# Performance work log

Hardware: AMD Instinct MI355X
Metric: run time of the kernel (lower is better)

## Reference

```python
import jax, jax.numpy as jnp
import numpy as np

EMB = 384
GROUPS = 4
B, T = 32, 1024
MAX_DUR = 8
SILENCE_VAL = -11.5129251


def setup_inputs() -> dict:
    key = jax.random.key(0)
    k1, k2, k3, k4, k5 = jax.random.split(key, 5)
    phoneme = jax.random.normal(k1, (B, T, EMB), dtype=jnp.float32)
    durations = jax.random.randint(k2, (B, T + 1), 0, MAX_DUR, dtype=jnp.int32)
    t_out = int(np.asarray(jnp.sum(durations, axis=-1)).max())
    silence_token = jnp.full((EMB,), SILENCE_VAL, dtype=jnp.float32)
    # DurationPredictor params (grouped conv -> ReLU -> 1x1 conv to scalar)
    conv1_w = jax.random.normal(k3, (EMB, EMB // GROUPS, 3), dtype=jnp.float32) * 0.05
    conv1_b = jnp.zeros((EMB,), dtype=jnp.float32)
    conv2_w = jax.random.normal(k4, (1, EMB, 1), dtype=jnp.float32) * 0.05
    conv2_b = jnp.zeros((1,), dtype=jnp.float32)
    return {
        "phoneme": phoneme,
        "silence_token": silence_token,
        "conv1_w": conv1_w,
        "conv1_b": conv1_b,
        "conv2_w": conv2_w,
        "conv2_b": conv2_b,
        "durations": durations,
        "t_out": t_out,
    }


def _duration_predictor(x, conv1_w, conv1_b, conv2_w, conv2_b):
    # x: [B, Tp, E] -> durations_pred [B, Tp]
    xc = jnp.transpose(x, (0, 2, 1))  # [B, E, Tp]
    h = jax.lax.conv_general_dilated(
        xc, conv1_w, window_strides=(1,), padding=((1, 1),),
        dimension_numbers=("NCH", "OIH", "NCH"), feature_group_count=GROUPS)
    h = jax.nn.relu(h + conv1_b[None, :, None])
    d = jax.lax.conv_general_dilated(
        h, conv2_w, window_strides=(1,), padding=((0, 0),),
        dimension_numbers=("NCH", "OIH", "NCH"))
    return d[:, 0, :] + conv2_b[0]  # [B, Tp]


def _regulate(phoneme, durations, t_out):
    # Equivalent to the one-hot mask matmul: frame t gets token j where
    # cumsum[j-1] <= t < cumsum[j]; frames past total length are zero.
    cum = jnp.cumsum(durations, axis=-1)  # [B, Tp]
    pos = jnp.arange(t_out, dtype=cum.dtype)  # [t_out]
    idx = jax.vmap(lambda c: jnp.searchsorted(c, pos, side="right"))(cum)  # [B, t_out]
    valid = pos[None, :] < cum[:, -1:]
    idx = jnp.clip(idx, 0, phoneme.shape[1] - 1)
    gathered = jnp.take_along_axis(phoneme, idx[..., None], axis=1)  # [B, t_out, E]
    return jnp.where(valid[..., None], gathered, jnp.zeros((), phoneme.dtype))


def reference(phoneme, silence_token, conv1_w, conv1_b, conv2_w, conv2_b, durations, t_out):
    Bn = phoneme.shape[0]
    silence = jnp.broadcast_to(silence_token[None, None, :], (Bn, 1, phoneme.shape[2]))
    ph = jnp.concatenate((phoneme, silence), axis=1)  # [B, T+1, E]
    durations_pred = _duration_predictor(ph, conv1_w, conv1_b, conv2_w, conv2_b)
    expanded = _regulate(ph, durations, t_out)  # [B, t_out, E]
    return expanded, durations_pred
```

## Files before the change

### kernel.cpp

```cpp
#include <hip/hip_runtime.h>

#define BATCH 32
#define T_IN 1024
#define TP 1025
#define EMB 384
#define GROUPS 4
#define GC 96
#define KDIM 288

typedef __attribute__((ext_vector_type(8))) short short8;
typedef __attribute__((ext_vector_type(4))) float f32x4;

#define N_WPACK (GROUPS * 9 * 6 * 64 * 8)

__device__ __forceinline__ unsigned short f2bf(float f) {
    union { float f; unsigned u; } v; v.f = f;
    unsigned u = v.u + 0x7fffu + ((v.u >> 16) & 1u);
    return (unsigned short)(u >> 16);
}

__global__ __launch_bounds__(256) void prep_kernel(const float* __restrict__ w1,
                                                   const float* __restrict__ b2,
                                                   unsigned short* __restrict__ wpack,
                                                   float* __restrict__ pred) {
    int i = blockIdx.x * 256 + threadIdx.x;
    if (i < N_WPACK) {
        int j = i & 7;
        int lane = (i >> 3) & 63;
        int rest = i >> 9;
        int nt = rest % 6; rest /= 6;
        int ks = rest % 9;
        int g = rest / 9;
        int oc = nt * 16 + (lane & 15);
        int kk = ks * 32 + (lane >> 4) * 8 + j;
        int k = kk / 96, ic = kk % 96;
        float v = w1[((size_t)(g * GC + oc) * GC + ic) * 3 + k];
        wpack[i] = f2bf(v);
    }
    if (i < BATCH * TP) pred[i] = b2[0];
}

__global__ __launch_bounds__(64) void scan_kernel(const int* __restrict__ dur,
                                                  int* __restrict__ cum) {
    const int b = blockIdx.x;
    const int l = threadIdx.x;
    const int* d = dur + b * TP;
    int* c = cum + b * TP;
    int offset = 0;
    for (int r = 0; r < 17; ++r) {
        int idx = r * 64 + l;
        int v = (idx < TP) ? d[idx] : 0;
        int s = v;
#pragma unroll
        for (int off = 1; off < 64; off <<= 1) {
            int n = __shfl_up(s, off, 64);
            if (l >= off) s += n;
        }
        if (idx < TP) c[idx] = s + offset;
        offset += __shfl(s, 63, 64);
    }
}

__global__ __launch_bounds__(256) void conv_mfma_kernel(const float* __restrict__ phoneme,
                                                        const float* __restrict__ silence,
                                                        const float* __restrict__ b1,
                                                        const float* __restrict__ w2,
                                                        const unsigned short* __restrict__ wpack,
                                                        float* __restrict__ pred) {
    const int tile = blockIdx.x;
    const int g = blockIdx.y;
    const int b = blockIdx.z;
    const int t0 = tile * 64;

    __shared__ __align__(16) unsigned short xs[66][104];
    __shared__ float red[4][16][17];

    const int tid = threadIdx.x;

    for (int e = tid; e < 66 * 24; e += 256) {
        int row = e / 24;
        int v = e - row * 24;
        int r = t0 - 1 + row;
        float4 val;
        if (r < 0 || r > T_IN) {
            val = make_float4(0.f, 0.f, 0.f, 0.f);
        } else if (r == T_IN) {
            val = *(const float4*)(silence + g * GC + v * 4);
        } else {
            val = *(const float4*)(phoneme + ((size_t)(b * T_IN + r)) * EMB + g * GC + v * 4);
        }
        ushort4 pk;
        pk.x = f2bf(val.x); pk.y = f2bf(val.y); pk.z = f2bf(val.z); pk.w = f2bf(val.w);
        *(ushort4*)&xs[row][v * 4] = pk;
    }
    __syncthreads();

    const int w = tid >> 6;
    const int lane = tid & 63;
    const int quad = lane >> 4;
    const int lr = lane & 15;

    f32x4 acc[6];
#pragma unroll
    for (int nt = 0; nt < 6; ++nt) acc[nt] = (f32x4){0.f, 0.f, 0.f, 0.f};

    const unsigned short* wg = wpack + (size_t)g * 9 * 6 * 512;

#pragma unroll
    for (int ks = 0; ks < 9; ++ks) {
        const int k = ks / 3;
        const int icoff = 32 * (ks % 3) + quad * 8;
        const int lrow = w * 16 + lr + k;
        short8 a = *(const short8*)&xs[lrow][icoff];
#pragma unroll
        for (int nt = 0; nt < 6; ++nt) {
            short8 bf = *(const short8*)(wg + ((size_t)(ks * 6 + nt) * 64 + lane) * 8);
            acc[nt] = __builtin_amdgcn_mfma_f32_16x16x32_bf16(a, bf, acc[nt], 0, 0, 0);
        }
    }

    float s[4] = {0.f, 0.f, 0.f, 0.f};
#pragma unroll
    for (int nt = 0; nt < 6; ++nt) {
        int oc = g * GC + nt * 16 + lr;
        float bias = b1[oc];
        float wc = w2[oc];
#pragma unroll
        for (int reg = 0; reg < 4; ++reg) {
            float h = acc[nt][reg] + bias;
            h = h > 0.f ? h : 0.f;
            s[reg] += wc * h;
        }
    }
#pragma unroll
    for (int reg = 0; reg < 4; ++reg) red[w][quad * 4 + reg][lr] = s[reg];
    __syncthreads();

    if (tid < 64) {
        int wv = tid >> 4, m = tid & 15;
        float sum = 0.f;
#pragma unroll
        for (int c2 = 0; c2 < 16; ++c2) sum += red[wv][m][c2];
        int t = t0 + wv * 16 + m;
        if (t < TP) atomicAdd(pred + b * TP + t, sum);
    }
}

__global__ __launch_bounds__(256) void gather_kernel(const float* __restrict__ phoneme,
                                                     const float* __restrict__ silence,
                                                     const int* __restrict__ cum,
                                                     float* __restrict__ out,
                                                     int t_out) {
    const int b = blockIdx.y;
    const int f0 = blockIdx.x * 64;
    const int tid = threadIdx.x;

    __shared__ int sidx[64];
    __shared__ int stotal;

    if (tid == 0) stotal = cum[b * TP + T_IN];
    if (tid < 64) {
        int t = f0 + tid;
        int id = 0;
        if (t < t_out) {
            const int* c = cum + b * TP;
            int lo = 0, hi = TP;
            while (lo < hi) {
                int mid = (lo + hi) >> 1;
                if (c[mid] <= t) lo = mid + 1; else hi = mid;
            }
            id = lo > T_IN ? T_IN : lo;
        }
        sidx[tid] = id;
    }
    __syncthreads();

    const int total = stotal;
    const float4* ph4 = (const float4*)phoneme;
    const float4* s4 = (const float4*)silence;
    float4* out4 = (float4*)out;

    for (int e = tid; e < 64 * 96; e += 256) {
        int fl = e / 96;
        int v = e - fl * 96;
        int t = f0 + fl;
        if (t >= t_out) continue;
        float4 val;
        if (t >= total) {
            val = make_float4(0.f, 0.f, 0.f, 0.f);
        } else {
            int id = sidx[fl];
            val = (id == T_IN) ? s4[v] : ph4[((size_t)(b * T_IN) + id) * 96 + v];
        }
        out4[((size_t)b * t_out + t) * 96 + v] = val;
    }
}

extern "C" void kernel_launch(void* const* d_in, const int* in_sizes, int n_in,
                              void* d_out, int out_size, void* d_ws, size_t ws_size,
                              hipStream_t stream) {
    const float* phoneme = (const float*)d_in[0];
    const float* silence = (const float*)d_in[1];
    const float* conv1_w = (const float*)d_in[2];
    const float* conv1_b = (const float*)d_in[3];
    const float* conv2_w = (const float*)d_in[4];
    const float* conv2_b = (const float*)d_in[5];
    const int* durations = (const int*)d_in[6];
    const int t_out = (out_size - BATCH * TP) / (BATCH * EMB);

    float* out_expanded = (float*)d_out;
    float* out_pred = (float*)d_out + (size_t)BATCH * t_out * EMB;

    int* cum = (int*)d_ws;
    unsigned short* wpack = (unsigned short*)((char*)d_ws + 131200);

    prep_kernel<<<(N_WPACK + 255) / 256, 256, 0, stream>>>(conv1_w, conv2_b, wpack, out_pred);
    scan_kernel<<<BATCH, 64, 0, stream>>>(durations, cum);
    conv_mfma_kernel<<<dim3(17, GROUPS, BATCH), 256, 0, stream>>>(
        phoneme, silence, conv1_b, conv2_w, wpack, out_pred);
    gather_kernel<<<dim3((t_out + 63) / 64, BATCH), 256, 0, stream>>>(
        phoneme, silence, cum, out_expanded, t_out);
}
```

Before: 263.3 us.

## Merge launches into setup and interleaved conv/gather kernel with nontemporal stores

Combines the weight-pack and scan kernels into one setup launch, and merges the conv and gather kernels into one launch whose blocks alternate between conv and gather work. This removes two kernel launches and lets compute-bound conv blocks overlap with bandwidth-bound gather blocks. The scan now preloads all of its duration values into registers before running, and the gather output uses nontemporal stores to avoid polluting the cache. The merged kernel reserves shared memory for both roles, which may lower occupancy.

```diff
diff --git a/kernel.cpp b/kernel.cpp
--- a/kernel.cpp
+++ b/kernel.cpp
@@ -12,6 +12,8 @@
 typedef __attribute__((ext_vector_type(4))) float f32x4;
 
 #define N_WPACK (GROUPS * 9 * 6 * 64 * 8)
+#define PREP_BLOCKS ((N_WPACK + 255) / 256)
+#define CONV_BLOCKS (17 * GROUPS * BATCH)
 
 __device__ __forceinline__ unsigned short f2bf(float f) {
     union { float f; unsigned u; } v; v.f = f;
@@ -19,180 +21,200 @@
     return (unsigned short)(u >> 16);
 }
 
-__global__ __launch_bounds__(256) void prep_kernel(const float* __restrict__ w1,
-                                                   const float* __restrict__ b2,
-                                                   unsigned short* __restrict__ wpack,
-                                                   float* __restrict__ pred) {
-    int i = blockIdx.x * 256 + threadIdx.x;
-    if (i < N_WPACK) {
-        int j = i & 7;
-        int lane = (i >> 3) & 63;
-        int rest = i >> 9;
-        int nt = rest % 6; rest /= 6;
-        int ks = rest % 9;
-        int g = rest / 9;
-        int oc = nt * 16 + (lane & 15);
-        int kk = ks * 32 + (lane >> 4) * 8 + j;
-        int k = kk / 96, ic = kk % 96;
-        float v = w1[((size_t)(g * GC + oc) * GC + ic) * 3 + k];
-        wpack[i] = f2bf(v);
+__global__ __launch_bounds__(256) void setup_kernel(const float* __restrict__ w1,
+                                                    const float* __restrict__ b2,
+                                                    const int* __restrict__ dur,
+                                                    unsigned short* __restrict__ wpack,
+                                                    float* __restrict__ pred,
+                                                    int* __restrict__ cum) {
+    const int bid = blockIdx.x;
+    if (bid < PREP_BLOCKS) {
+        int i = bid * 256 + threadIdx.x;
+        if (i < N_WPACK) {
+            int j = i & 7;
+            int lane = (i >> 3) & 63;
+            int rest = i >> 9;
+            int nt = rest % 6; rest /= 6;
+            int ks = rest % 9;
+            int g = rest / 9;
+            int oc = nt * 16 + (lane & 15);
+            int kk = ks * 32 + (lane >> 4) * 8 + j;
+            int k = kk / 96, ic = kk % 96;
+            float v = w1[((size_t)(g * GC + oc) * GC + ic) * 3 + k];
+            wpack[i] = f2bf(v);
+        }
+        if (i < BATCH * TP) pred[i] = b2[0];
+    } else {
+        const int b = bid - PREP_BLOCKS;
+        const int l = threadIdx.x;
+        if (l >= 64) return;
+        const int* d = dur + b * TP;
+        int* c = cum + b * TP;
+        int v[17];
+#pragma unroll
+        for (int r = 0; r < 17; ++r) {
+            int idx = r * 64 + l;
+            v[r] = (idx < TP) ? d[idx] : 0;
+        }
+        int offset = 0;
+#pragma unroll
+        for (int r = 0; r < 17; ++r) {
+            int s = v[r];
+#pragma unroll
+            for (int off = 1; off < 64; off <<= 1) {
+                int n = __shfl_up(s, off, 64);
+                if (l >= off) s += n;
+            }
+            int idx = r * 64 + l;
+            if (idx < TP) c[idx] = s + offset;
+            offset += __shfl(s, 63, 64);
+        }
     }
-    if (i < BATCH * TP) pred[i] = b2[0];
-}
-
-__global__ __launch_bounds__(64) void scan_kernel(const int* __restrict__ dur,
-                                                  int* __restrict__ cum) {
-    const int b = blockIdx.x;
-    const int l = threadIdx.x;
-    const int* d = dur + b * TP;
-    int* c = cum + b * TP;
-    int offset = 0;
-    for (int r = 0; r < 17; ++r) {
-        int idx = r * 64 + l;
-        int v = (idx < TP) ? d[idx] : 0;
-        int s = v;
-#pragma unroll
-        for (int off = 1; off < 64; off <<= 1) {
-            int n = __shfl_up(s, off, 64);
-            if (l >= off) s += n;
-        }
-        if (idx < TP) c[idx] = s + offset;
-        offset += __shfl(s, 63, 64);
-    }
-}
-
-__global__ __launch_bounds__(256) void conv_mfma_kernel(const float* __restrict__ phoneme,
-                                                        const float* __restrict__ silence,
-                                                        const float* __restrict__ b1,
-                                                        const float* __restrict__ w2,
-                                                        const unsigned short* __restrict__ wpack,
-                                                        float* __restrict__ pred) {
-    const int tile = blockIdx.x;
-    const int g = blockIdx.y;
-    const int b = blockIdx.z;
-    const int t0 = tile * 64;
-
+}
+
+__global__ __launch_bounds__(256) void main_kernel(const float* __restrict__ phoneme,
+                                                   const float* __restrict__ silence,
+                                                   const float* __restrict__ b1,
+                                                   const float* __restrict__ w2,
+                                                   const unsigned short* __restrict__ wpack,
+                                                   const int* __restrict__ cum,
+                                                   float* __restrict__ pred,
+                                                   float* __restrict__ out,
+                                                   int t_out, int nfb, int n_gather) {
     __shared__ __align__(16) unsigned short xs[66][104];
     __shared__ float red[4][16][17];
-
-    const int tid = threadIdx.x;
-
-    for (int e = tid; e < 66 * 24; e += 256) {
-        int row = e / 24;
-        int v = e - row * 24;
-        int r = t0 - 1 + row;
-        float4 val;
-        if (r < 0 || r > T_IN) {
-            val = make_float4(0.f, 0.f, 0.f, 0.f);
-        } else if (r == T_IN) {
-            val = *(const float4*)(silence + g * GC + v * 4);
-        } else {
-            val = *(const float4*)(phoneme + ((size_t)(b * T_IN + r)) * EMB + g * GC + v * 4);
-        }
-        ushort4 pk;
-        pk.x = f2bf(val.x); pk.y = f2bf(val.y); pk.z = f2bf(val.z); pk.w = f2bf(val.w);
-        *(ushort4*)&xs[row][v * 4] = pk;
-    }
-    __syncthreads();
-
-    const int w = tid >> 6;
-    const int lane = tid & 63;
-    const int quad = lane >> 4;
-    const int lr = lane & 15;
-
-    f32x4 acc[6];
-#pragma unroll
-    for (int nt = 0; nt < 6; ++nt) acc[nt] = (f32x4){0.f, 0.f, 0.f, 0.f};
-
-    const unsigned short* wg = wpack + (size_t)g * 9 * 6 * 512;
-
-#pragma unroll
-    for (int ks = 0; ks < 9; ++ks) {
-        const int k = ks / 3;
-        const int icoff = 32 * (ks % 3) + quad * 8;
-        const int lrow = w * 16 + lr + k;
-        short8 a = *(const short8*)&xs[lrow][icoff];
-#pragma unroll
-        for (int nt = 0; nt < 6; ++nt) {
-            short8 bf = *(const short8*)(wg + ((size_t)(ks * 6 + nt) * 64 + lane) * 8);
-            acc[nt] = __builtin_amdgcn_mfma_f32_16x16x32_bf16(a, bf, acc[nt], 0, 0, 0);
-        }
-    }
-
-    float s[4] = {0.f, 0.f, 0.f, 0.f};
-#pragma unroll
-    for (int nt = 0; nt < 6; ++nt) {
-        int oc = g * GC + nt * 16 + lr;
-        float bias = b1[oc];
-        float wc = w2[oc];
-#pragma unroll
-        for (int reg = 0; reg < 4; ++reg) {
-            float h = acc[nt][reg] + bias;
-            h = h > 0.f ? h : 0.f;
-            s[reg] += wc * h;
-        }
-    }
-#pragma unroll
-    for (int reg = 0; reg < 4; ++reg) red[w][quad * 4 + reg][lr] = s[reg];
-    __syncthreads();
-
-    if (tid < 64) {
-        int wv = tid >> 4, m = tid & 15;
-        float sum = 0.f;
-#pragma unroll
-        for (int c2 = 0; c2 < 16; ++c2) sum += red[wv][m][c2];
-        int t = t0 + wv * 16 + m;
-        if (t < TP) atomicAdd(pred + b * TP + t, sum);
-    }
-}
-
-__global__ __launch_bounds__(256) void gather_kernel(const float* __restrict__ phoneme,
-                                                     const float* __restrict__ silence,
-                                                     const int* __restrict__ cum,
-                                                     float* __restrict__ out,
-                                                     int t_out) {
-    const int b = blockIdx.y;
-    const int f0 = blockIdx.x * 64;
-    const int tid = threadIdx.x;
-
     __shared__ int sidx[64];
     __shared__ int stotal;
 
-    if (tid == 0) stotal = cum[b * TP + T_IN];
-    if (tid < 64) {
-        int t = f0 + tid;
-        int id = 0;
-        if (t < t_out) {
-            const int* c = cum + b * TP;
-            int lo = 0, hi = TP;
-            while (lo < hi) {
-                int mid = (lo + hi) >> 1;
-                if (c[mid] <= t) lo = mid + 1; else hi = mid;
-            }
-            id = lo > T_IN ? T_IN : lo;
-        }
-        sidx[tid] = id;
+    const int bid = blockIdx.x;
+    const int nc = CONV_BLOCKS;
+    const int ng = n_gather;
+    const int mn = nc < ng ? nc : ng;
+    bool isConv;
+    int sub;
+    if (bid < 2 * mn) {
+        isConv = (bid & 1);
+        sub = bid >> 1;
+    } else {
+        isConv = (nc > ng);
+        sub = mn + (bid - 2 * mn);
     }
-    __syncthreads();
-
-    const int total = stotal;
-    const float4* ph4 = (const float4*)phoneme;
-    const float4* s4 = (const float4*)silence;
-    float4* out4 = (float4*)out;
-
-    for (int e = tid; e < 64 * 96; e += 256) {
-        int fl = e / 96;
-        int v = e - fl * 96;
-        int t = f0 + fl;
-        if (t >= t_out) continue;
-        float4 val;
-        if (t >= total) {
-            val = make_float4(0.f, 0.f, 0.f, 0.f);
-        } else {
-            int id = sidx[fl];
-            val = (id == T_IN) ? s4[v] : ph4[((size_t)(b * T_IN) + id) * 96 + v];
-        }
-        out4[((size_t)b * t_out + t) * 96 + v] = val;
+
+    const int tid = threadIdx.x;
+
+    if (isConv) {
+        const int tile = sub % 17;
+        const int g = (sub / 17) & 3;
+        const int b = sub / (17 * 4);
+        const int t0 = tile * 64;
+
+        for (int e = tid; e < 66 * 24; e += 256) {
+            int row = e / 24;
+            int v = e - row * 24;
+            int r = t0 - 1 + row;
+            f32x4 val;
+            if (r < 0 || r > T_IN) {
+                val = (f32x4){0.f, 0.f, 0.f, 0.f};
+            } else if (r == T_IN) {
+                val = *(const f32x4*)(silence + g * GC + v * 4);
+            } else {
+                val = *(const f32x4*)(phoneme + ((size_t)(b * T_IN + r)) * EMB + g * GC + v * 4);
+            }
+            ushort4 pk;
+            pk.x = f2bf(val.x); pk.y = f2bf(val.y); pk.z = f2bf(val.z); pk.w = f2bf(val.w);
+            *(ushort4*)&xs[row][v * 4] = pk;
+        }
+        __syncthreads();
+
+        const int w = tid >> 6;
+        const int lane = tid & 63;
+        const int quad = lane >> 4;
+        const int lr = lane & 15;
+
+        f32x4 acc[6];
+#pragma unroll
+        for (int nt = 0; nt < 6; ++nt) acc[nt] = (f32x4){0.f, 0.f, 0.f, 0.f};
+
+        const unsigned short* wg = wpack + (size_t)g * 9 * 6 * 512;
+
+#pragma unroll
+        for (int ks = 0; ks < 9; ++ks) {
+            const int k = ks / 3;
+            const int icoff = 32 * (ks % 3) + quad * 8;
+            const int lrow = w * 16 + lr + k;
+            short8 a = *(const short8*)&xs[lrow][icoff];
+#pragma unroll
+            for (int nt = 0; nt < 6; ++nt) {
+                short8 bf = *(const short8*)(wg + ((size_t)(ks * 6 + nt) * 64 + lane) * 8);
+                acc[nt] = __builtin_amdgcn_mfma_f32_16x16x32_bf16(a, bf, acc[nt], 0, 0, 0);
+            }
+        }
+
+        float s[4] = {0.f, 0.f, 0.f, 0.f};
+#pragma unroll
+        for (int nt = 0; nt < 6; ++nt) {
+            int oc = g * GC + nt * 16 + lr;
+            float bias = b1[oc];
+            float wc = w2[oc];
+#pragma unroll
+            for (int reg = 0; reg < 4; ++reg) {
+                float h = acc[nt][reg] + bias;
+                h = h > 0.f ? h : 0.f;
+                s[reg] += wc * h;
+            }
+        }
+#pragma unroll
+        for (int reg = 0; reg < 4; ++reg) red[w][quad * 4 + reg][lr] = s[reg];
+        __syncthreads();
+
+        if (tid < 64) {
+            int wv = tid >> 4, m = tid & 15;
+            float sum = 0.f;
+#pragma unroll
+            for (int c2 = 0; c2 < 16; ++c2) sum += red[wv][m][c2];
+            int t = t0 + wv * 16 + m;
+            if (t < TP) atomicAdd(pred + b * TP + t, sum);
+        }
+    } else {
+        const int b = sub / nfb;
+        const int f0 = (sub - b * nfb) * 64;
+
+        if (tid == 0) stotal = cum[b * TP + T_IN];
+        if (tid < 64) {
+            int t = f0 + tid;
+            int id = 0;
+            if (t < t_out) {
+                const int* c = cum + b * TP;
+                int lo = 0, hi = TP;
+                while (lo < hi) {
+                    int mid = (lo + hi) >> 1;
+                    if (c[mid] <= t) lo = mid + 1; else hi = mid;
+                }
+                id = lo > T_IN ? T_IN : lo;
+            }
+            sidx[tid] = id;
+        }
+        __syncthreads();
+
+        const int total = stotal;
+        const f32x4* ph4 = (const f32x4*)phoneme;
+        const f32x4* s4 = (const f32x4*)silence;
+        f32x4* out4 = (f32x4*)out;
+
+        for (int e = tid; e < 64 * 96; e += 256) {
+            int fl = e / 96;
+            int v = e - fl * 96;
+            int t = f0 + fl;
+            if (t >= t_out) continue;
+            f32x4 val;
+            if (t >= total) {
+                val = (f32x4){0.f, 0.f, 0.f, 0.f};
+            } else {
+                int id = sidx[fl];
+                val = (id == T_IN) ? s4[v] : ph4[((size_t)(b * T_IN) + id) * 96 + v];
+            }
+            __builtin_nontemporal_store(val, &out4[((size_t)b * t_out + t) * 96 + v]);
+        }
     }
 }
 
@@ -214,10 +236,12 @@
     int* cum = (int*)d_ws;
     unsigned short* wpack = (unsigned short*)((char*)d_ws + 131200);
 
-    prep_kernel<<<(N_WPACK + 255) / 256, 256, 0, stream>>>(conv1_w, conv2_b, wpack, out_pred);
-    scan_kernel<<<BATCH, 64, 0, stream>>>(durations, cum);
-    conv_mfma_kernel<<<dim3(17, GROUPS, BATCH), 256, 0, stream>>>(
-        phoneme, silence, conv1_b, conv2_w, wpack, out_pred);
-    gather_kernel<<<dim3((t_out + 63) / 64, BATCH), 256, 0, stream>>>(
-        phoneme, silence, cum, out_expanded, t_out);
-}
+    const int nfb = (t_out + 63) / 64;
+    const int n_gather = nfb * BATCH;
+
+    setup_kernel<<<PREP_BLOCKS + BATCH, 256, 0, stream>>>(
+        conv1_w, conv2_b, durations, wpack, out_pred, cum);
+    main_kernel<<<CONV_BLOCKS + n_gather, 256, 0, stream>>>(
+        phoneme, silence, conv1_b, conv2_w, wpack, cum, out_pred, out_expanded,
+        t_out, nfb, n_gather);
+}
```

After: 262.6 us. Within noise of the previous version (-0.3%).
